# Performance work log

Hardware: AMD Instinct MI355X
Metric: run time of the kernel (lower is better)

The kernel has to match this reference:

```python
import jax, jax.numpy as jnp
import numpy as np

N_NODES = 100000
N_EDGES = 800000
IN_DIM = 64
HID = 96
OUT_DIM = 1
N_LAYERS = 3
N_CENTRAL = 512
BN_EPS = 1e-5


def setup_inputs() -> dict:
    key = jax.random.key(0)
    ks = jax.random.split(key, 16)
    s = 0.1  # weight scale to keep activations tame
    return {
        "x": jax.random.normal(ks[0], (N_NODES, IN_DIM), jnp.float32),
        "edge_index": jax.random.randint(ks[1], (2, N_EDGES), 0, N_NODES, jnp.int64 if jax.config.jax_enable_x64 else jnp.int32),
        "batch": jnp.zeros((N_NODES,), jnp.int32),
        "central_node_idx": jax.random.randint(ks[2], (N_CENTRAL,), 0, N_NODES, jnp.int32),
        "W_emb": jax.random.normal(ks[3], (IN_DIM, HID), jnp.float32) * s,
        "b_emb": jax.random.normal(ks[4], (HID,), jnp.float32) * s,
        "conv_wl": jax.random.normal(ks[5], (N_LAYERS, HID, HID), jnp.float32) * s,
        "conv_bl": jax.random.normal(ks[6], (N_LAYERS, HID), jnp.float32) * s,
        "conv_wr": jax.random.normal(ks[7], (N_LAYERS, HID, HID), jnp.float32) * s,
        "bn_gamma": jnp.ones((N_LAYERS, HID), jnp.float32),
        "bn_beta": jnp.zeros((N_LAYERS, HID), jnp.float32),
        "W1": jax.random.normal(ks[8], (HID, HID), jnp.float32) * s,
        "b1": jax.random.normal(ks[9], (HID,), jnp.float32) * s,
        "W2": jax.random.normal(ks[10], (HID, OUT_DIM), jnp.float32) * s,
        "b2": jax.random.normal(ks[11], (OUT_DIM,), jnp.float32) * s,
    }


def _sage_mean_agg(h, src, dst, n):
    # PyG SAGEConv mean aggregation: mean of source features at each target node
    msg = h[src]                                             # [E, H] gather
    summed = jax.ops.segment_sum(msg, dst, num_segments=n)   # [N, H] scatter-add
    deg = jax.ops.segment_sum(jnp.ones((src.shape[0],), h.dtype), dst, num_segments=n)
    return summed / jnp.maximum(deg, 1.0)[:, None]


def reference(x, edge_index, batch, central_node_idx, W_emb, b_emb,
              conv_wl, conv_bl, conv_wr, bn_gamma, bn_beta, W1, b1, W2, b2):
    n = x.shape[0]
    src, dst = edge_index[0], edge_index[1]
    h = jax.nn.relu(x @ W_emb + b_emb)                       # [N, H]
    for i in range(conv_wl.shape[0]):
        agg = _sage_mean_agg(h, src, dst, n)
        # SAGEConv: lin_l(agg) (with bias) + lin_r(x_root) (no bias)
        h = agg @ conv_wl[i] + conv_bl[i] + h @ conv_wr[i]
        # BatchNorm1d, training mode: batch stats with biased variance
        mean = h.mean(axis=0)
        var = h.var(axis=0)
        h = (h - mean) * jax.lax.rsqrt(var + BN_EPS) * bn_gamma[i] + bn_beta[i]
        h = jax.nn.relu(h)
    central = h[central_node_idx]                            # [G, H]
    out = jax.nn.relu(central @ W1 + b1) @ W2 + b2           # [G, OUT]
    return out
```

## Files before the change

kernel.cpp:

```cpp
#include <hip/hip_runtime.h>

#define NN 100000
#define NE 800000
#define IND 64
#define HID 96
#define NL 3
#define NC 512
#define BN_EPS 1e-5f

#define NBE ((NN + 127) / 128)
#define NBP (NL * 9)
#define NBH ((NE + 4095) / 4096)

typedef __attribute__((ext_vector_type(8))) short bf16x8;
typedef __attribute__((ext_vector_type(4))) float f32x4;

static __device__ __forceinline__ float b2f(ushort u) {
    union { uint i; float f; } v; v.i = ((uint)u) << 16; return v.f;
}
static __device__ __forceinline__ ushort f2b(float f) {
    union { float f; uint i; } v; v.f = f;
    uint r = v.i + 0x7FFFu + ((v.i >> 16) & 1u);
    return (ushort)(r >> 16);
}
static __device__ __forceinline__ uint pack2(float a, float b) {
    return (uint)f2b(a) | ((uint)f2b(b) << 16);
}

static __device__ __forceinline__ void prep_one(const float* srcA, const float* srcB,
                                                ushort* dst, int t) {
    int lane = t & 63;
    int ct = (t >> 6) % 6;
    int kt = t / (6 * 64);
    int k0 = kt * 32 + (lane >> 4) * 8;
    int col = ct * 16 + (lane & 15);
    ushort tmp[8];
#pragma unroll
    for (int j = 0; j < 8; ++j) {
        int k = k0 + j;
        const float* src = (srcB == nullptr || k < 96) ? srcA : srcB;
        int kk = (srcB == nullptr || k < 96) ? k : k - 96;
        tmp[j] = f2b(src[kk * HID + col]);
    }
    uint* od = (uint*)(dst + (size_t)t * 8);
    od[0] = (uint)tmp[0] | ((uint)tmp[1] << 16);
    od[1] = (uint)tmp[2] | ((uint)tmp[3] << 16);
    od[2] = (uint)tmp[4] | ((uint)tmp[5] << 16);
    od[3] = (uint)tmp[6] | ((uint)tmp[7] << 16);
}

__global__ __launch_bounds__(256) void k_front(const float* __restrict__ x,
        const float* __restrict__ W_emb, const float* __restrict__ bias,
        ushort* __restrict__ h,
        const float* __restrict__ conv_wl, const float* __restrict__ conv_wr,
        ushort* __restrict__ Bfl,
        const int* __restrict__ ei, int* __restrict__ hist) {
    const int b = blockIdx.x;
    const int tid = threadIdx.x;
    if (b >= NBE) {
        if (b < NBE + NBP) {
            int idx = b - NBE;
            int l = idx / 9, bb = idx % 9;
            int t = bb * 256 + tid;
            if (t < 6 * 6 * 64)
                prep_one(conv_wl + (size_t)l * 9216, conv_wr + (size_t)l * 9216,
                         Bfl + (size_t)l * 18432, t);
        } else {
            int base = (b - NBE - NBP) * 4096;
            for (int i = tid; i < 4096; i += 256) {
                int e = base + i;
                if (e < NE) atomicAdd(&hist[ei[NE + e]], 1);
            }
        }
        return;
    }
    __shared__ __align__(16) char smem[24576];
    ushort* sB = (ushort*)smem;
    ushort* sT = (ushort*)smem;
    for (int i = tid; i < 768; i += 256) {
        int lane = i & 63;
        int ct = (i >> 6) % 6;
        int kt = i / (6 * 64);
        int k0 = kt * 32 + (lane >> 4) * 8;
        int col = ct * 16 + (lane & 15);
        ushort tmp[8];
#pragma unroll
        for (int j = 0; j < 8; ++j) tmp[j] = f2b(W_emb[(k0 + j) * HID + col]);
        uint4 o;
        o.x = (uint)tmp[0] | ((uint)tmp[1] << 16);
        o.y = (uint)tmp[2] | ((uint)tmp[3] << 16);
        o.z = (uint)tmp[4] | ((uint)tmp[5] << 16);
        o.w = (uint)tmp[6] | ((uint)tmp[7] << 16);
        ((uint4*)sB)[i] = o;
    }
    __syncthreads();
    const int wave = tid >> 6, lane = tid & 63;
    const int rowb = wave * 32;
    const int row0 = b * 128 + rowb;
    const int kof = (lane >> 4) * 8;
    f32x4 acc[2][6];
#pragma unroll
    for (int t = 0; t < 2; ++t)
#pragma unroll
        for (int c = 0; c < 6; ++c) acc[t][c] = (f32x4){0.f, 0.f, 0.f, 0.f};
#pragma unroll
    for (int kt = 0; kt < 2; ++kt) {
        int kk = kt * 32 + kof;
        bf16x8 a[2];
#pragma unroll
        for (int t = 0; t < 2; ++t) {
            int r = row0 + t * 16 + (lane & 15);
            if (r >= NN) r = NN - 1;
            const float* src = x + (size_t)r * IND + kk;
            float4 f0 = *(const float4*)src;
            float4 f1 = *(const float4*)(src + 4);
            a[t][0] = (short)f2b(f0.x); a[t][1] = (short)f2b(f0.y);
            a[t][2] = (short)f2b(f0.z); a[t][3] = (short)f2b(f0.w);
            a[t][4] = (short)f2b(f1.x); a[t][5] = (short)f2b(f1.y);
            a[t][6] = (short)f2b(f1.z); a[t][7] = (short)f2b(f1.w);
        }
#pragma unroll
        for (int ct = 0; ct < 6; ++ct) {
            bf16x8 bb = *(const bf16x8*)&sB[((kt * 6 + ct) * 64 + lane) * 8];
            acc[0][ct] = __builtin_amdgcn_mfma_f32_16x16x32_bf16(a[0], bb, acc[0][ct], 0, 0, 0);
            acc[1][ct] = __builtin_amdgcn_mfma_f32_16x16x32_bf16(a[1], bb, acc[1][ct], 0, 0, 0);
        }
    }
    __syncthreads();
#pragma unroll
    for (int t = 0; t < 2; ++t)
#pragma unroll
        for (int ct = 0; ct < 6; ++ct) {
            int col = ct * 16 + (lane & 15);
            float bv = bias[col];
#pragma unroll
            for (int i = 0; i < 4; ++i) {
                int rb = rowb + t * 16 + (lane >> 4) * 4 + i;
                float v = acc[t][ct][i] + bv;
                sT[rb * HID + col] = f2b(v > 0.f ? v : 0.f);
            }
        }
    __syncthreads();
    for (int i = tid; i < 1536; i += 256) {
        int r = i / 12;
        int g = b * 128 + r;
        if (g < NN) ((uint4*)(h + (size_t)g * HID))[i % 12] = ((uint4*)sT)[i];
    }
}

__global__ __launch_bounds__(1024) void k_scan1(const int* __restrict__ hist,
        int* __restrict__ rp, int* __restrict__ bsum) {
    __shared__ int sd[1024];
    const int tid = threadIdx.x;
    const int i = blockIdx.x * 1024 + tid;
    int v = (i < NN) ? hist[i] : 0;
    sd[tid] = v;
    __syncthreads();
    for (int off = 1; off < 1024; off <<= 1) {
        int t = (tid >= off) ? sd[tid - off] : 0;
        __syncthreads();
        sd[tid] += t;
        __syncthreads();
    }
    if (i < NN) rp[i] = sd[tid] - v;
    if (tid == 1023) bsum[blockIdx.x] = sd[1023];
}

__global__ __launch_bounds__(128) void k_scan2(const int* __restrict__ bsum,
                                               int* __restrict__ boff) {
    __shared__ int sd[128];
    const int tid = threadIdx.x;
    const int NB = (NN + 1023) / 1024;
    int v = (tid < NB) ? bsum[tid] : 0;
    sd[tid] = v;
    __syncthreads();
    for (int off = 1; off < 128; off <<= 1) {
        int t = (tid >= off) ? sd[tid - off] : 0;
        __syncthreads();
        sd[tid] += t;
        __syncthreads();
    }
    if (tid < NB) boff[tid] = sd[tid] - v;
}

__global__ __launch_bounds__(1024) void k_scan3(int* __restrict__ rp,
        const int* __restrict__ boff, int* __restrict__ curs) {
    const int i = blockIdx.x * 1024 + threadIdx.x;
    if (i < NN) {
        int v = rp[i] + boff[blockIdx.x];
        rp[i] = v;
        curs[i] = v;
    }
    if (i == 0) rp[NN] = NE;
}

__global__ void k_fill(const int* __restrict__ ei, int* __restrict__ cursor,
                       int* __restrict__ col) {
    int e = blockIdx.x * blockDim.x + threadIdx.x;
    if (e < NE) {
        int d = ei[NE + e];
        int pos = atomicAdd(&cursor[d], 1);
        col[pos] = ei[e];
    }
}

__global__ __launch_bounds__(256) void k_agg(const ushort* __restrict__ pre,
        const int* __restrict__ rp, const int* __restrict__ col,
        const float* __restrict__ stats, const float* __restrict__ gamma,
        const float* __restrict__ beta, ushort* __restrict__ agg) {
    __shared__ float sc[96], sh[96];
    const int tid = threadIdx.x;
    if (tid < 96) {
        float scv = 1.f, shv = 0.f;
        if (stats) {
            float mean = stats[tid] * (1.f / NN);
            float var  = stats[96 + tid] * (1.f / NN) - mean * mean;
            float s = gamma[tid] * rsqrtf(var + BN_EPS);
            scv = s; shv = beta[tid] - mean * s;
        }
        sc[tid] = scv; sh[tid] = shv;
    }
    __syncthreads();
    const int lane = tid & 15;
    const int n = blockIdx.x * 16 + (tid >> 4);
    if (n >= NN) return;
    const float s0a = sc[2*lane],      h0a = sh[2*lane];
    const float s0b = sc[2*lane + 1],  h0b = sh[2*lane + 1];
    const float s1a = sc[2*lane + 32], h1a = sh[2*lane + 32];
    const float s1b = sc[2*lane + 33], h1b = sh[2*lane + 33];
    const float s2a = sc[2*lane + 64], h2a = sh[2*lane + 64];
    const float s2b = sc[2*lane + 65], h2b = sh[2*lane + 65];
    const int e0 = rp[n], e1 = rp[n + 1];
    float a0 = 0.f, a1 = 0.f, a2 = 0.f, a3 = 0.f, a4 = 0.f, a5 = 0.f;
    const uint* hu = (const uint*)pre;
    int e = e0;
    for (; e + 8 <= e1; e += 8) {
        uint u[8][3];
#pragma unroll
        for (int i = 0; i < 8; ++i) {
            const uint* r = hu + (size_t)col[e + i] * 48 + lane;
            u[i][0] = r[0]; u[i][1] = r[16]; u[i][2] = r[32];
        }
#pragma unroll
        for (int i = 0; i < 8; ++i) {
            a0 += fmaxf(b2f((ushort)u[i][0])         * s0a + h0a, 0.f);
            a1 += fmaxf(b2f((ushort)(u[i][0] >> 16)) * s0b + h0b, 0.f);
            a2 += fmaxf(b2f((ushort)u[i][1])         * s1a + h1a, 0.f);
            a3 += fmaxf(b2f((ushort)(u[i][1] >> 16)) * s1b + h1b, 0.f);
            a4 += fmaxf(b2f((ushort)u[i][2])         * s2a + h2a, 0.f);
            a5 += fmaxf(b2f((ushort)(u[i][2] >> 16)) * s2b + h2b, 0.f);
        }
    }
    for (; e + 4 <= e1; e += 4) {
        uint u[4][3];
#pragma unroll
        for (int i = 0; i < 4; ++i) {
            const uint* r = hu + (size_t)col[e + i] * 48 + lane;
            u[i][0] = r[0]; u[i][1] = r[16]; u[i][2] = r[32];
        }
#pragma unroll
        for (int i = 0; i < 4; ++i) {
            a0 += fmaxf(b2f((ushort)u[i][0])         * s0a + h0a, 0.f);
            a1 += fmaxf(b2f((ushort)(u[i][0] >> 16)) * s0b + h0b, 0.f);
            a2 += fmaxf(b2f((ushort)u[i][1])         * s1a + h1a, 0.f);
            a3 += fmaxf(b2f((ushort)(u[i][1] >> 16)) * s1b + h1b, 0.f);
            a4 += fmaxf(b2f((ushort)u[i][2])         * s2a + h2a, 0.f);
            a5 += fmaxf(b2f((ushort)(u[i][2] >> 16)) * s2b + h2b, 0.f);
        }
    }
    for (; e < e1; ++e) {
        const uint* r = hu + (size_t)col[e] * 48 + lane;
        uint u0 = r[0], u1 = r[16], u2 = r[32];
        a0 += fmaxf(b2f((ushort)u0)         * s0a + h0a, 0.f);
        a1 += fmaxf(b2f((ushort)(u0 >> 16)) * s0b + h0b, 0.f);
        a2 += fmaxf(b2f((ushort)u1)         * s1a + h1a, 0.f);
        a3 += fmaxf(b2f((ushort)(u1 >> 16)) * s1b + h1b, 0.f);
        a4 += fmaxf(b2f((ushort)u2)         * s2a + h2a, 0.f);
        a5 += fmaxf(b2f((ushort)(u2 >> 16)) * s2b + h2b, 0.f);
    }
    int d = e1 - e0; if (d < 1) d = 1;
    float inv = 1.0f / (float)d;
    uint* ar = (uint*)agg + (size_t)n * 48 + lane;
    ar[0]  = pack2(a0 * inv, a1 * inv);
    ar[16] = pack2(a2 * inv, a3 * inv);
    ar[32] = pack2(a4 * inv, a5 * inv);
}

__global__ __launch_bounds__(256, 4) void k_gemm(const ushort* __restrict__ aggb,
        const ushort* __restrict__ pre, const ushort* __restrict__ Bf,
        const float* __restrict__ bl, ushort* __restrict__ hnew,
        float* __restrict__ stats,
        const float* __restrict__ statsP, const float* __restrict__ gammaP,
        const float* __restrict__ betaP) {
    __shared__ __align__(16) char smem[40704];
    ushort* sB = (ushort*)smem;
    ushort* sT = (ushort*)smem;
    float*  sredS = (float*)(smem + 36864);
    float*  sredQ = (float*)(smem + 38400);
    float2* sscsh = (float2*)(smem + 39936);
    const int tid = threadIdx.x;
    for (int i = tid; i < 2304; i += 256) ((uint4*)sB)[i] = ((const uint4*)Bf)[i];
    if (tid < 96) {
        float scv = 1.f, shv = 0.f;
        if (statsP) {
            float mean = statsP[tid] * (1.f / NN);
            float var  = statsP[96 + tid] * (1.f / NN) - mean * mean;
            float s = gammaP[tid] * rsqrtf(var + BN_EPS);
            scv = s; shv = betaP[tid] - mean * s;
        }
        sscsh[tid] = make_float2(scv, shv);
    }
    __syncthreads();
    const int wave = tid >> 6, lane = tid & 63;
    const int rowb = wave * 32;
    const int row0 = blockIdx.x * 128 + rowb;
    const int kof = (lane >> 4) * 8;
    f32x4 acc[2][6];
#pragma unroll
    for (int t = 0; t < 2; ++t)
#pragma unroll
        for (int c = 0; c < 6; ++c) acc[t][c] = (f32x4){0.f, 0.f, 0.f, 0.f};
#pragma unroll
    for (int kt = 0; kt < 6; ++kt) {
        bf16x8 a[2];
#pragma unroll
        for (int t = 0; t < 2; ++t) {
            int r = row0 + t * 16 + (lane & 15);
            if (r >= NN) r = NN - 1;
            if (kt < 3) {
                int kk = kt * 32 + kof;
                a[t] = *(const bf16x8*)(aggb + (size_t)r * HID + kk);
            } else {
                int kk = (kt - 3) * 32 + kof;
                bf16x8 raw = *(const bf16x8*)(pre + (size_t)r * HID + kk);
                union { bf16x8 h; uint u[4]; } pk;
#pragma unroll
                for (int j = 0; j < 4; ++j) {
                    float2 p0 = sscsh[kk + 2*j];
                    float2 p1 = sscsh[kk + 2*j + 1];
                    float v0 = fmaxf(b2f((ushort)raw[2*j])     * p0.x + p0.y, 0.f);
                    float v1 = fmaxf(b2f((ushort)raw[2*j + 1]) * p1.x + p1.y, 0.f);
                    pk.u[j] = pack2(v0, v1);
                }
                a[t] = pk.h;
            }
        }
#pragma unroll
        for (int ct = 0; ct < 6; ++ct) {
            bf16x8 bb = *(const bf16x8*)&sB[((kt * 6 + ct) * 64 + lane) * 8];
            acc[0][ct] = __builtin_amdgcn_mfma_f32_16x16x32_bf16(a[0], bb, acc[0][ct], 0, 0, 0);
            acc[1][ct] = __builtin_amdgcn_mfma_f32_16x16x32_bf16(a[1], bb, acc[1][ct], 0, 0, 0);
        }
    }
    __syncthreads();
    float s[6], q[6];
#pragma unroll
    for (int c = 0; c < 6; ++c) { s[c] = 0.f; q[c] = 0.f; }
#pragma unroll
    for (int t = 0; t < 2; ++t)
#pragma unroll
        for (int ct = 0; ct < 6; ++ct) {
            int col = ct * 16 + (lane & 15);
            float bv = bl[col];
#pragma unroll
            for (int i = 0; i < 4; ++i) {
                int rb = rowb + t * 16 + (lane >> 4) * 4 + i;
                int g = blockIdx.x * 128 + rb;
                float v = acc[t][ct][i] + bv;
                if (g < NN) { s[ct] += v; q[ct] += v * v; }
                sT[rb * HID + col] = f2b(v);
            }
        }
#pragma unroll
    for (int c = 0; c < 6; ++c) {
        s[c] += __shfl_xor(s[c], 16); s[c] += __shfl_xor(s[c], 32);
        q[c] += __shfl_xor(q[c], 16); q[c] += __shfl_xor(q[c], 32);
    }
    if (lane < 16) {
#pragma unroll
        for (int c = 0; c < 6; ++c) {
            sredS[wave * 96 + c * 16 + lane] = s[c];
            sredQ[wave * 96 + c * 16 + lane] = q[c];
        }
    }
    __syncthreads();
    if (tid < 96) {
        float S = sredS[tid] + sredS[96 + tid] + sredS[192 + tid] + sredS[288 + tid];
        float Q = sredQ[tid] + sredQ[96 + tid] + sredQ[192 + tid] + sredQ[288 + tid];
        atomicAdd(&stats[tid], S);
        atomicAdd(&stats[96 + tid], Q);
    }
    for (int i = tid; i < 1536; i += 256) {
        int r = i / 12;
        int g = blockIdx.x * 128 + r;
        if (g < NN) ((uint4*)(hnew + (size_t)g * HID))[i % 12] = ((uint4*)sT)[i];
    }
}

__global__ __launch_bounds__(128) void k_mlp(const ushort* __restrict__ pre,
        const int* __restrict__ cidx, const float* __restrict__ stats,
        const float* __restrict__ gamma, const float* __restrict__ beta,
        const float* __restrict__ W1, const float* __restrict__ b1,
        const float* __restrict__ W2, const float* __restrict__ b2,
        float* __restrict__ out) {
    __shared__ float nh[96];
    __shared__ float hid[96];
    __shared__ float red[128];
    const int c = blockIdx.x;
    const int node = cidx[c];
    const int tid = threadIdx.x;
    if (tid < 96) {
        float mean = stats[tid] * (1.f / NN);
        float var  = stats[96 + tid] * (1.f / NN) - mean * mean;
        float s = gamma[tid] * rsqrtf(var + BN_EPS);
        float v = b2f(pre[(size_t)node * 96 + tid]) * s + (beta[tid] - mean * s);
        nh[tid] = fmaxf(v, 0.f);
    }
    __syncthreads();
    if (tid < 96) {
        float a = 0.f;
        for (int k = 0; k < 96; ++k) a += nh[k] * W1[k * 96 + tid];
        hid[tid] = fmaxf(a + b1[tid], 0.f);
    }
    __syncthreads();
    red[tid] = (tid < 96) ? hid[tid] * W2[tid] : 0.f;
    __syncthreads();
    for (int off = 64; off > 0; off >>= 1) {
        if (tid < off) red[tid] += red[tid + off];
        __syncthreads();
    }
    if (tid == 0) out[c] = red[0] + b2[0];
}

extern "C" void kernel_launch(void* const* d_in, const int* in_sizes, int n_in,
                              void* d_out, int out_size, void* d_ws, size_t ws_size,
                              hipStream_t stream) {
    const float* x        = (const float*)d_in[0];
    const int*   ei       = (const int*)d_in[1];
    const int*   cidx     = (const int*)d_in[3];
    const float* W_emb    = (const float*)d_in[4];
    const float* b_emb    = (const float*)d_in[5];
    const float* conv_wl  = (const float*)d_in[6];
    const float* conv_bl  = (const float*)d_in[7];
    const float* conv_wr  = (const float*)d_in[8];
    const float* bn_gamma = (const float*)d_in[9];
    const float* bn_beta  = (const float*)d_in[10];
    const float* W1       = (const float*)d_in[11];
    const float* b1       = (const float*)d_in[12];
    const float* W2       = (const float*)d_in[13];
    const float* b2       = (const float*)d_in[14];
    float* out = (float*)d_out;

    char* ws = (char*)d_ws;
    size_t off = 0;
    auto alloc = [&](size_t bytes) -> void* {
        void* p = ws + off;
        off = (off + bytes + 255) & ~(size_t)255;
        return p;
    };
    ushort* h    = (ushort*)alloc((size_t)NN * 96 * 2);
    ushort* hnew = (ushort*)alloc((size_t)NN * 96 * 2);
    ushort* agg  = (ushort*)alloc((size_t)NN * 96 * 2);
    int*   hist  = (int*)alloc((size_t)NN * 4);
    int*   rp    = (int*)alloc((size_t)(NN + 1) * 4);
    int*   curs  = (int*)alloc((size_t)NN * 4);
    int*   col   = (int*)alloc((size_t)NE * 4);
    int*   bsum  = (int*)alloc(128 * 4);
    int*   boff  = (int*)alloc(128 * 4);
    float* stats = (float*)alloc((size_t)NL * 192 * 4);
    ushort* Bfl  = (ushort*)alloc((size_t)NL * 6 * 6 * 64 * 8 * 2);
    (void)ws_size; (void)in_sizes; (void)n_in; (void)out_size;

    const int NB = (NN + 1023) / 1024;

    hipMemsetAsync(hist, 0, (size_t)NN * 4, stream);
    hipMemsetAsync(stats, 0, (size_t)NL * 192 * 4, stream);

    k_front<<<NBE + NBP + NBH, 256, 0, stream>>>(x, W_emb, b_emb, h,
        conv_wl, conv_wr, Bfl, ei, hist);
    k_scan1<<<NB, 1024, 0, stream>>>(hist, rp, bsum);
    k_scan2<<<1, 128, 0, stream>>>(bsum, boff);
    k_scan3<<<NB, 1024, 0, stream>>>(rp, boff, curs);
    k_fill<<<(NE + 255) / 256, 256, 0, stream>>>(ei, curs, col);

    const ushort* src = h;
    ushort* dst = hnew;
    for (int l = 0; l < NL; ++l) {
        const float* stP = (l == 0) ? nullptr : stats + (size_t)(l - 1) * 192;
        const float* gP  = (l == 0) ? nullptr : bn_gamma + (size_t)(l - 1) * 96;
        const float* bP  = (l == 0) ? nullptr : bn_beta + (size_t)(l - 1) * 96;
        k_agg<<<(NN + 15) / 16, 256, 0, stream>>>(src, rp, col, stP, gP, bP, agg);
        k_gemm<<<(NN + 127) / 128, 256, 0, stream>>>(agg, src,
            Bfl + (size_t)l * 18432, conv_bl + (size_t)l * 96, dst,
            stats + (size_t)l * 192, stP, gP, bP);
        const ushort* t = src; src = dst; dst = (ushort*)t;
    }
    k_mlp<<<NC, 128, 0, stream>>>(src, cidx, stats + (size_t)(NL - 1) * 192,
        bn_gamma + (size_t)(NL - 1) * 96, bn_beta + (size_t)(NL - 1) * 96,
        W1, b1, W2, b2, out);
}
```

Before: 299.0 us.

## Replace global-atomic CSR fill with two-level bucketed partition and LDS-atomic fill

Measured after the change: 271.9 us. -9.1%, faster.

```diff
diff --git a/kernel.cpp b/kernel.cpp
--- a/kernel.cpp
+++ b/kernel.cpp
@@ -11,6 +11,9 @@
 #define NBE ((NN + 127) / 128)
 #define NBP (NL * 9)
 #define NBH ((NE + 4095) / 4096)
+#define NBF ((NE + 4095) / 4096)
+#define NBK2 196
+#define BCAP 4864
 
 typedef __attribute__((ext_vector_type(8))) short bf16x8;
 typedef __attribute__((ext_vector_type(4))) float f32x4;
@@ -54,7 +57,9 @@
         ushort* __restrict__ h,
         const float* __restrict__ conv_wl, const float* __restrict__ conv_wr,
         ushort* __restrict__ Bfl,
-        const int* __restrict__ ei, int* __restrict__ hist) {
+        const int* __restrict__ ei, int* __restrict__ hist,
+        int* __restrict__ gcur, uint* __restrict__ part) {
+    __shared__ __align__(16) char smem[24576];
     const int b = blockIdx.x;
     const int tid = threadIdx.x;
     if (b >= NBE) {
@@ -65,16 +70,63 @@
             if (t < 6 * 6 * 64)
                 prep_one(conv_wl + (size_t)l * 9216, conv_wr + (size_t)l * 9216,
                          Bfl + (size_t)l * 18432, t);
-        } else {
+        } else if (b < NBE + NBP + NBH) {
             int base = (b - NBE - NBP) * 4096;
             for (int i = tid; i < 4096; i += 256) {
                 int e = base + i;
                 if (e < NE) atomicAdd(&hist[ei[NE + e]], 1);
             }
+        } else {
+            uint* ordbuf = (uint*)smem;
+            unsigned char* sbk = (unsigned char*)(smem + 16384);
+            int* lhist = (int*)(smem + 20480);
+            int* lscan = (int*)(smem + 21504);
+            int* lbase = (int*)(smem + 22528);
+            int* lcnt2 = (int*)(smem + 23552);
+            const int base_e = (b - NBE - NBP - NBH) * 4096;
+            lhist[tid] = 0; lcnt2[tid] = 0;
+            __syncthreads();
+#pragma unroll
+            for (int it = 0; it < 16; ++it) {
+                int e = base_e + it * 256 + tid;
+                if (e < NE) atomicAdd(&lhist[ei[NE + e] >> 9], 1);
+            }
+            __syncthreads();
+            int v = lhist[tid];
+            lscan[tid] = v;
+            __syncthreads();
+            for (int off = 1; off < 256; off <<= 1) {
+                int t2 = (tid >= off) ? lscan[tid - off] : 0;
+                __syncthreads();
+                lscan[tid] += t2;
+                __syncthreads();
+            }
+            int excl = lscan[tid] - v;
+            __syncthreads();
+            lscan[tid] = excl;
+            if (v > 0) lbase[tid] = atomicAdd(&gcur[tid], v);
+            __syncthreads();
+#pragma unroll
+            for (int it = 0; it < 16; ++it) {
+                int e = base_e + it * 256 + tid;
+                if (e < NE) {
+                    int s = ei[e], d = ei[NE + e];
+                    int bk = d >> 9;
+                    int lofs = atomicAdd(&lcnt2[bk], 1);
+                    int slot = lscan[bk] + lofs;
+                    ordbuf[slot] = (uint)s | ((uint)(d & 511) << 17);
+                    sbk[slot] = (unsigned char)bk;
+                }
+            }
+            __syncthreads();
+            int total = NE - base_e; if (total > 4096) total = 4096;
+            for (int i = tid; i < total; i += 256) {
+                int bk = sbk[i];
+                part[(size_t)bk * BCAP + lbase[bk] + (i - lscan[bk])] = ordbuf[i];
+            }
         }
         return;
     }
-    __shared__ __align__(16) char smem[24576];
     ushort* sB = (ushort*)smem;
     ushort* sT = (ushort*)smem;
     for (int i = tid; i < 768; i += 256) {
@@ -184,23 +236,30 @@
 }
 
 __global__ __launch_bounds__(1024) void k_scan3(int* __restrict__ rp,
-        const int* __restrict__ boff, int* __restrict__ curs) {
+        const int* __restrict__ boff) {
     const int i = blockIdx.x * 1024 + threadIdx.x;
-    if (i < NN) {
-        int v = rp[i] + boff[blockIdx.x];
-        rp[i] = v;
-        curs[i] = v;
-    }
+    if (i < NN) rp[i] += boff[blockIdx.x];
     if (i == 0) rp[NN] = NE;
 }
 
-__global__ void k_fill(const int* __restrict__ ei, int* __restrict__ cursor,
-                       int* __restrict__ col) {
-    int e = blockIdx.x * blockDim.x + threadIdx.x;
-    if (e < NE) {
-        int d = ei[NE + e];
-        int pos = atomicAdd(&cursor[d], 1);
-        col[pos] = ei[e];
+__global__ __launch_bounds__(256) void k_fill2(const uint* __restrict__ part,
+        const int* __restrict__ gcur, const int* __restrict__ rp,
+        int* __restrict__ col) {
+    __shared__ int lcur[512];
+    const int tid = threadIdx.x;
+    const int bk = blockIdx.x;
+    const int n0 = bk * 512;
+    for (int i = tid; i < 512; i += 256) {
+        int n = n0 + i;
+        lcur[i] = (n < NN) ? rp[n] : 0;
+    }
+    __syncthreads();
+    const int cnt = gcur[bk];
+    const uint* pb = part + (size_t)bk * BCAP;
+    for (int e = tid; e < cnt; e += 256) {
+        uint v = pb[e];
+        int pos = atomicAdd(&lcur[v >> 17], 1);
+        col[pos] = (int)(v & 0x1FFFF);
     }
 }
 
@@ -462,9 +521,10 @@
     ushort* hnew = (ushort*)alloc((size_t)NN * 96 * 2);
     ushort* agg  = (ushort*)alloc((size_t)NN * 96 * 2);
     int*   hist  = (int*)alloc((size_t)NN * 4);
+    int*   gcur  = (int*)alloc(256 * 4);
     int*   rp    = (int*)alloc((size_t)(NN + 1) * 4);
-    int*   curs  = (int*)alloc((size_t)NN * 4);
     int*   col   = (int*)alloc((size_t)NE * 4);
+    uint*  part  = (uint*)alloc((size_t)NBK2 * BCAP * 4);
     int*   bsum  = (int*)alloc(128 * 4);
     int*   boff  = (int*)alloc(128 * 4);
     float* stats = (float*)alloc((size_t)NL * 192 * 4);
@@ -473,15 +533,15 @@
 
     const int NB = (NN + 1023) / 1024;
 
-    hipMemsetAsync(hist, 0, (size_t)NN * 4, stream);
+    hipMemsetAsync(hist, 0, ((size_t)NN * 4 + 255 & ~(size_t)255) + 256 * 4, stream);
     hipMemsetAsync(stats, 0, (size_t)NL * 192 * 4, stream);
 
-    k_front<<<NBE + NBP + NBH, 256, 0, stream>>>(x, W_emb, b_emb, h,
-        conv_wl, conv_wr, Bfl, ei, hist);
+    k_front<<<NBE + NBP + NBH + NBF, 256, 0, stream>>>(x, W_emb, b_emb, h,
+        conv_wl, conv_wr, Bfl, ei, hist, gcur, part);
     k_scan1<<<NB, 1024, 0, stream>>>(hist, rp, bsum);
     k_scan2<<<1, 128, 0, stream>>>(bsum, boff);
-    k_scan3<<<NB, 1024, 0, stream>>>(rp, boff, curs);
-    k_fill<<<(NE + 255) / 256, 256, 0, stream>>>(ei, curs, col);
+    k_scan3<<<NB, 1024, 0, stream>>>(rp, boff);
+    k_fill2<<<NBK2, 256, 0, stream>>>(part, gcur, rp, col);
 
     const ushort* src = h;
     ushort* dst = hnew;
```
